# Performance work log

Measured on AMD Instinct MI355X. Metric: run time of the kernel, lower is better.

The kernel has to match this reference:

```python
import jax, jax.numpy as jnp
import numpy as np

N_DOWN, N_ABOVE, D_IN, D_OUT, FAN_IN = 50000, 100000, 256, 256, 5


def setup_inputs() -> dict:
    key = jax.random.key(0)
    ks = jax.random.split(key, 8)
    h = jax.random.normal(ks[0], (N_DOWN, D_IN), dtype=jnp.float32)
    h_above = jax.random.normal(ks[1], (N_ABOVE, D_IN), dtype=jnp.float32)  # only shape[0] used
    # idx: unique positions of the down nodes within the up-node index space
    idx = jax.random.permutation(ks[2], N_ABOVE)[:N_DOWN]
    # fixed fan-in 5: destination ids i are each node repeated 5 times (DGL bucketing order)
    i = jnp.repeat(jnp.arange(N_ABOVE), FAN_IN)
    j = jax.random.randint(ks[3], (N_ABOVE * FAN_IN,), 0, N_ABOVE)
    s1 = 1.0 / np.sqrt(D_IN * FAN_IN)
    s2 = 1.0 / np.sqrt(D_OUT)
    W1 = jax.random.uniform(ks[4], (D_IN * FAN_IN, D_OUT), jnp.float32, -s1, s1)
    b1 = jax.random.uniform(ks[5], (D_OUT,), jnp.float32, -s1, s1)
    W2 = jax.random.uniform(ks[6], (D_OUT, D_OUT), jnp.float32, -s2, s2)
    b2 = jax.random.uniform(ks[7], (D_OUT,), jnp.float32, -s2, s2)
    return {"h": h, "h_above": h_above, "idx": idx, "i": i, "j": j,
            "W1": W1, "b1": b1, "W2": W2, "b2": b2}


def reference(h, h_above, idx, i, j, W1, b1, W2, b2):
    n_above = h_above.shape[0]
    d = h.shape[1]
    # scatter down-node features into the up-node index space (new_h[idx] = h)
    new_h = jnp.zeros((n_above, d), dtype=h.dtype).at[idx].set(h)
    # gather the 5 source-node messages per destination; i = repeat(arange, 5),
    # so j grouped in blocks of 5 corresponds to each destination's mailbox.
    gathered = new_h[j].reshape(n_above, 5 * d)  # [n_above, 5*d]
    hid = jax.nn.relu(gathered @ W1 + b1)
    return hid @ W2 + b2
```

## Files before the change

kernel.cpp:

```cpp
#include <hip/hip_runtime.h>

#define N_DOWN  50000
#define N_ABOVE 100000
#define DIM     256
#define FAN     5
#define K1      1280
#define MPAD    100096

typedef __bf16 bf16x8 __attribute__((ext_vector_type(8)));
typedef float  f32x4  __attribute__((ext_vector_type(4)));

__device__ __forceinline__ unsigned short f2bf(float f) {
  unsigned u = __builtin_bit_cast(unsigned, f);
  u += 0x7FFFu + ((u >> 16) & 1u);
  return (unsigned short)(u >> 16);
}

__device__ __forceinline__ void gload16(const unsigned short* g, unsigned short* l) {
  __builtin_amdgcn_global_load_lds(
      (const __attribute__((address_space(1))) void*)g,
      (__attribute__((address_space(3))) void*)l, 16, 0, 0);
}

__global__ void k_prep_inv(int* __restrict__ inv, unsigned short* __restrict__ hbf) {
  int t = blockIdx.x * 256 + threadIdx.x;
  if (t < N_ABOVE) inv[t] = N_DOWN;
  if (t < DIM)     hbf[(size_t)N_DOWN * DIM + t] = 0;
}

__global__ void k_scatter(const int* __restrict__ idx, int* __restrict__ inv) {
  int t = blockIdx.x * 256 + threadIdx.x;
  if (t < N_DOWN) inv[idx[t]] = t;
}

__global__ void k_h2bf(const float* __restrict__ h, unsigned short* __restrict__ hbf) {
  int t = blockIdx.x * 256 + threadIdx.x;
  float4 v = ((const float4*)h)[t];
  ushort4 o;
  o.x = f2bf(v.x); o.y = f2bf(v.y); o.z = f2bf(v.z); o.w = f2bf(v.w);
  ((ushort4*)hbf)[t] = o;
}

__global__ void k_transpose_bf(const float* __restrict__ in, unsigned short* __restrict__ out,
                               int K, int N) {
  __shared__ float tile[64][65];
  int k0 = blockIdx.x * 64, n0 = blockIdx.y * 64;
  int c = threadIdx.x & 63, rb = threadIdx.x >> 6;
#pragma unroll
  for (int rr = 0; rr < 16; ++rr) {
    int row = rb + rr * 4;
    tile[row][c] = in[(size_t)(k0 + row) * N + n0 + c];
  }
  __syncthreads();
#pragma unroll
  for (int rr = 0; rr < 16; ++rr) {
    int nr = rb + rr * 4;
    out[(size_t)(n0 + nr) * K + k0 + c] = f2bf(tile[c][nr]);
  }
}

__global__ __launch_bounds__(256, 2) void k_gemm1(
    const unsigned short* __restrict__ hbf,
    const unsigned short* __restrict__ w1t,
    const float* __restrict__ b1,
    const int* __restrict__ inv,
    const int* __restrict__ jarr,
    unsigned short* __restrict__ hid)
{
  __shared__ __align__(16) unsigned short Alds[128 * 64];
  __shared__ __align__(16) unsigned short Blds[128 * 64];
  __shared__ int srcrow[128 * FAN];

  const int tid = threadIdx.x;
  const int w = tid >> 6, l = tid & 63;
  const int m0 = blockIdx.x * 128, n0 = blockIdx.y * 128;
  const int wm = w >> 1, wn = w & 1;
  const int srow = l >> 3, slot = l & 7;

  for (int e = tid; e < 128 * FAN; e += 256) {
    int row = e / FAN, rr = e - row * FAN;
    int gm = m0 + row;
    int s = N_DOWN;
    if (gm < N_ABOVE) s = inv[jarr[(size_t)gm * FAN + rr]];
    srcrow[e] = s;
  }

  f32x4 acc[4][4] = {};

  for (int t = 0; t < 20; ++t) {
    const int r = t >> 2;
    __syncthreads();
#pragma unroll
    for (int i = 0; i < 4; ++i) {
      int row = w * 32 + i * 8 + srow;
      int src = srcrow[row * FAN + r];
      int c = slot ^ (row & 7);
      gload16(hbf + ((size_t)src << 8) + ((t & 3) << 6) + (c << 3),
              Alds + (w * 32 + i * 8) * 64);
    }
#pragma unroll
    for (int i = 0; i < 4; ++i) {
      int row = w * 32 + i * 8 + srow;
      int c = slot ^ (row & 7);
      gload16(w1t + (size_t)(n0 + row) * K1 + (t << 6) + (c << 3),
              Blds + (w * 32 + i * 8) * 64);
    }
    __syncthreads();

#pragma unroll
    for (int kk = 0; kk < 2; ++kk) {
      bf16x8 af[4], bfr[4];
#pragma unroll
      for (int m = 0; m < 4; ++m) {
        int row = wm * 64 + m * 16 + (l & 15);
        int c = (kk * 4 + (l >> 4)) ^ (row & 7);
        af[m] = *(const bf16x8*)(Alds + row * 64 + c * 8);
      }
#pragma unroll
      for (int n = 0; n < 4; ++n) {
        int row = wn * 64 + n * 16 + (l & 15);
        int c = (kk * 4 + (l >> 4)) ^ (row & 7);
        bfr[n] = *(const bf16x8*)(Blds + row * 64 + c * 8);
      }
#pragma unroll
      for (int m = 0; m < 4; ++m)
#pragma unroll
        for (int n = 0; n < 4; ++n)
          acc[m][n] = __builtin_amdgcn_mfma_f32_16x16x32_bf16(af[m], bfr[n], acc[m][n], 0, 0, 0);
    }
  }

#pragma unroll
  for (int n = 0; n < 4; ++n) {
    int gn = n0 + wn * 64 + n * 16 + (l & 15);
    float bias = b1[gn];
#pragma unroll
    for (int m = 0; m < 4; ++m) {
      int gm0 = m0 + wm * 64 + m * 16 + (l >> 4) * 4;
#pragma unroll
      for (int q = 0; q < 4; ++q) {
        float v = acc[m][n][q] + bias;
        v = v > 0.f ? v : 0.f;
        hid[(size_t)(gm0 + q) * DIM + gn] = f2bf(v);
      }
    }
  }
}

__global__ __launch_bounds__(256, 2) void k_gemm2(
    const unsigned short* __restrict__ hid,
    const unsigned short* __restrict__ w2t,
    const float* __restrict__ b2,
    float* __restrict__ out)
{
  __shared__ __align__(16) unsigned short Alds[128 * 64];
  __shared__ __align__(16) unsigned short Blds[128 * 64];

  const int tid = threadIdx.x;
  const int w = tid >> 6, l = tid & 63;
  const int m0 = blockIdx.x * 128, n0 = blockIdx.y * 128;
  const int wm = w >> 1, wn = w & 1;
  const int srow = l >> 3, slot = l & 7;

  f32x4 acc[4][4] = {};

  for (int t = 0; t < 4; ++t) {
    __syncthreads();
#pragma unroll
    for (int i = 0; i < 4; ++i) {
      int row = w * 32 + i * 8 + srow;
      int c = slot ^ (row & 7);
      gload16(hid + (size_t)(m0 + row) * DIM + (t << 6) + (c << 3),
              Alds + (w * 32 + i * 8) * 64);
      gload16(w2t + (size_t)(n0 + row) * DIM + (t << 6) + (c << 3),
              Blds + (w * 32 + i * 8) * 64);
    }
    __syncthreads();

#pragma unroll
    for (int kk = 0; kk < 2; ++kk) {
      bf16x8 af[4], bfr[4];
#pragma unroll
      for (int m = 0; m < 4; ++m) {
        int row = wm * 64 + m * 16 + (l & 15);
        int c = (kk * 4 + (l >> 4)) ^ (row & 7);
        af[m] = *(const bf16x8*)(Alds + row * 64 + c * 8);
      }
#pragma unroll
      for (int n = 0; n < 4; ++n) {
        int row = wn * 64 + n * 16 + (l & 15);
        int c = (kk * 4 + (l >> 4)) ^ (row & 7);
        bfr[n] = *(const bf16x8*)(Blds + row * 64 + c * 8);
      }
#pragma unroll
      for (int m = 0; m < 4; ++m)
#pragma unroll
        for (int n = 0; n < 4; ++n)
          acc[m][n] = __builtin_amdgcn_mfma_f32_16x16x32_bf16(af[m], bfr[n], acc[m][n], 0, 0, 0);
    }
  }

#pragma unroll
  for (int n = 0; n < 4; ++n) {
    int gn = n0 + wn * 64 + n * 16 + (l & 15);
    float bias = b2[gn];
#pragma unroll
    for (int m = 0; m < 4; ++m) {
      int gm0 = m0 + wm * 64 + m * 16 + (l >> 4) * 4;
#pragma unroll
      for (int q = 0; q < 4; ++q) {
        int gm = gm0 + q;
        if (gm < N_ABOVE) out[(size_t)gm * DIM + gn] = acc[m][n][q] + bias;
      }
    }
  }
}

extern "C" void kernel_launch(void* const* d_in, const int* in_sizes, int n_in,
                              void* d_out, int out_size, void* d_ws, size_t ws_size,
                              hipStream_t stream) {
  const float* h    = (const float*)d_in[0];
  const int*   idx  = (const int*)d_in[2];
  const int*   jarr = (const int*)d_in[4];
  const float* W1   = (const float*)d_in[5];
  const float* b1   = (const float*)d_in[6];
  const float* W2   = (const float*)d_in[7];
  const float* b2   = (const float*)d_in[8];
  float* out = (float*)d_out;

  char* ws = (char*)d_ws;
  size_t off = 0;
  auto alloc = [&](size_t bytes) -> void* {
    void* p = ws + off;
    off += bytes;
    off = (off + 511) & ~(size_t)511;
    return p;
  };
  int*            inv = (int*)alloc((size_t)N_ABOVE * 4);
  unsigned short* hbf = (unsigned short*)alloc((size_t)(N_DOWN + 1) * DIM * 2);
  unsigned short* w1t = (unsigned short*)alloc((size_t)DIM * K1 * 2);
  unsigned short* w2t = (unsigned short*)alloc((size_t)DIM * DIM * 2);
  unsigned short* hid = (unsigned short*)alloc((size_t)MPAD * DIM * 2);
  if (ws_size < off) return;

  k_prep_inv<<<dim3(391), dim3(256), 0, stream>>>(inv, hbf);
  k_scatter<<<dim3(196), dim3(256), 0, stream>>>(idx, inv);
  k_h2bf<<<dim3(12500), dim3(256), 0, stream>>>(h, hbf);
  k_transpose_bf<<<dim3(K1 / 64, DIM / 64), dim3(256), 0, stream>>>(W1, w1t, K1, DIM);
  k_transpose_bf<<<dim3(DIM / 64, DIM / 64), dim3(256), 0, stream>>>(W2, w2t, DIM, DIM);
  k_gemm1<<<dim3(MPAD / 128, 2), dim3(256), 0, stream>>>(hbf, w1t, b1, inv, jarr, hid);
  k_gemm2<<<dim3(MPAD / 128, 2), dim3(256), 0, stream>>>(hid, w2t, b2, out);
}
```

Measured before the change: 142.8 us.

## Restructure gemm1 with 128x256 tiles, 512 threads and triple-buffered async pipeline

Rewrites the first GEMM so each block covers the full 256-wide output with 8 waves, which halves the number of gathers of the indexed A rows. It triple-buffers LDS and prefetches two K-tiles ahead using direct-to-LDS loads with explicit vmcnt waits. MFMA phases are interleaved with half-tile LDS reads and raised wave priority. The source indices are held in registers instead of LDS. This uses about 147KB of dynamic shared memory per block, which limits occupancy, and it relies on hand-placed waitcnt and barrier ordering for correctness.

```diff
diff --git a/kernel.cpp b/kernel.cpp
--- a/kernel.cpp
+++ b/kernel.cpp
@@ -6,6 +6,7 @@
 #define FAN     5
 #define K1      1280
 #define MPAD    100096
+#define NT      20
 
 typedef __bf16 bf16x8 __attribute__((ext_vector_type(8)));
 typedef float  f32x4  __attribute__((ext_vector_type(4)));
@@ -21,6 +22,10 @@
       (const __attribute__((address_space(1))) void*)g,
       (__attribute__((address_space(3))) void*)l, 16, 0, 0);
 }
+
+#define BAR()   __builtin_amdgcn_s_barrier()
+#define LGKM0() do { asm volatile("s_waitcnt lgkmcnt(0)" ::: "memory"); \
+                     __builtin_amdgcn_sched_barrier(0); } while (0)
 
 __global__ void k_prep_inv(int* __restrict__ inv, unsigned short* __restrict__ hbf) {
   int t = blockIdx.x * 256 + threadIdx.x;
@@ -59,7 +64,7 @@
   }
 }
 
-__global__ __launch_bounds__(256, 2) void k_gemm1(
+__global__ __launch_bounds__(512, 2) void k_gemm1(
     const unsigned short* __restrict__ hbf,
     const unsigned short* __restrict__ w1t,
     const float* __restrict__ b1,
@@ -67,81 +72,147 @@
     const int* __restrict__ jarr,
     unsigned short* __restrict__ hid)
 {
-  __shared__ __align__(16) unsigned short Alds[128 * 64];
-  __shared__ __align__(16) unsigned short Blds[128 * 64];
-  __shared__ int srcrow[128 * FAN];
+  extern __shared__ __align__(16) unsigned short smem[];
+  unsigned short* As = smem;
+  unsigned short* Bs = smem + 3 * 128 * 64;
 
   const int tid = threadIdx.x;
   const int w = tid >> 6, l = tid & 63;
-  const int m0 = blockIdx.x * 128, n0 = blockIdx.y * 128;
-  const int wm = w >> 1, wn = w & 1;
-  const int srow = l >> 3, slot = l & 7;
-
-  for (int e = tid; e < 128 * FAN; e += 256) {
-    int row = e / FAN, rr = e - row * FAN;
-    int gm = m0 + row;
-    int s = N_DOWN;
-    if (gm < N_ABOVE) s = inv[jarr[(size_t)gm * FAN + rr]];
-    srcrow[e] = s;
-  }
+  const int m0 = blockIdx.x * 128;
+  const int wm = w & 1, wn = w >> 1;
+  const int la = l >> 3, lc = l & 7;
+
+  const int rA0 = w * 16 + la;
+  const int rA1 = w * 16 + 8 + la;
+  const int cA0 = lc ^ (rA0 & 7);
+  const int cA1 = lc ^ (rA1 & 7);
+  const int rB0 = w * 32 + la,      cB0 = lc ^ (rB0 & 7);
+  const int rB1 = w * 32 + 8 + la,  cB1 = lc ^ (rB1 & 7);
+  const int rB2 = w * 32 + 16 + la, cB2 = lc ^ (rB2 & 7);
+  const int rB3 = w * 32 + 24 + la, cB3 = lc ^ (rB3 & 7);
+
+  const int gm0 = min(m0 + rA0, N_ABOVE - 1);
+  const int gm1 = min(m0 + rA1, N_ABOVE - 1);
+  const int s00 = inv[jarr[gm0 * FAN + 0]], s01 = inv[jarr[gm0 * FAN + 1]],
+            s02 = inv[jarr[gm0 * FAN + 2]], s03 = inv[jarr[gm0 * FAN + 3]],
+            s04 = inv[jarr[gm0 * FAN + 4]];
+  const int s10 = inv[jarr[gm1 * FAN + 0]], s11 = inv[jarr[gm1 * FAN + 1]],
+            s12 = inv[jarr[gm1 * FAN + 2]], s13 = inv[jarr[gm1 * FAN + 3]],
+            s14 = inv[jarr[gm1 * FAN + 4]];
+  asm volatile("s_waitcnt vmcnt(0)" ::: "memory");
+  __builtin_amdgcn_sched_barrier(0);
+
+#pragma unroll
+  for (int t = 0; t < 2; ++t) {
+    unsigned short* An = As + t * (128 * 64);
+    unsigned short* Bn = Bs + t * (256 * 64);
+    int u = t >> 2;
+    (void)u;
+    int a0 = (t == 0) ? s00 : s00;
+    int a1 = (t == 0) ? s10 : s10;
+    gload16(hbf + ((size_t)a0 << 8) + ((t & 3) << 6) + (cA0 << 3), An + (w * 2 + 0) * 512);
+    gload16(hbf + ((size_t)a1 << 8) + ((t & 3) << 6) + (cA1 << 3), An + (w * 2 + 1) * 512);
+    gload16(w1t + (size_t)rB0 * K1 + (t << 6) + (cB0 << 3), Bn + (w * 4 + 0) * 512);
+    gload16(w1t + (size_t)rB1 * K1 + (t << 6) + (cB1 << 3), Bn + (w * 4 + 1) * 512);
+    gload16(w1t + (size_t)rB2 * K1 + (t << 6) + (cB2 << 3), Bn + (w * 4 + 2) * 512);
+    gload16(w1t + (size_t)rB3 * K1 + (t << 6) + (cB3 << 3), Bn + (w * 4 + 3) * 512);
+  }
+  asm volatile("s_waitcnt vmcnt(6)" ::: "memory");
+  BAR();
 
   f32x4 acc[4][4] = {};
-
-  for (int t = 0; t < 20; ++t) {
-    const int r = t >> 2;
-    __syncthreads();
-#pragma unroll
-    for (int i = 0; i < 4; ++i) {
-      int row = w * 32 + i * 8 + srow;
-      int src = srcrow[row * FAN + r];
-      int c = slot ^ (row & 7);
-      gload16(hbf + ((size_t)src << 8) + ((t & 3) << 6) + (c << 3),
-              Alds + (w * 32 + i * 8) * 64);
-    }
-#pragma unroll
-    for (int i = 0; i < 4; ++i) {
-      int row = w * 32 + i * 8 + srow;
-      int c = slot ^ (row & 7);
-      gload16(w1t + (size_t)(n0 + row) * K1 + (t << 6) + (c << 3),
-              Blds + (w * 32 + i * 8) * 64);
-    }
-    __syncthreads();
-
-#pragma unroll
-    for (int kk = 0; kk < 2; ++kk) {
-      bf16x8 af[4], bfr[4];
-#pragma unroll
-      for (int m = 0; m < 4; ++m) {
-        int row = wm * 64 + m * 16 + (l & 15);
-        int c = (kk * 4 + (l >> 4)) ^ (row & 7);
-        af[m] = *(const bf16x8*)(Alds + row * 64 + c * 8);
-      }
-#pragma unroll
-      for (int n = 0; n < 4; ++n) {
-        int row = wn * 64 + n * 16 + (l & 15);
-        int c = (kk * 4 + (l >> 4)) ^ (row & 7);
-        bfr[n] = *(const bf16x8*)(Blds + row * 64 + c * 8);
-      }
-#pragma unroll
-      for (int m = 0; m < 4; ++m)
-#pragma unroll
-        for (int n = 0; n < 4; ++n)
-          acc[m][n] = __builtin_amdgcn_mfma_f32_16x16x32_bf16(af[m], bfr[n], acc[m][n], 0, 0, 0);
-    }
-  }
-
-#pragma unroll
-  for (int n = 0; n < 4; ++n) {
-    int gn = n0 + wn * 64 + n * 16 + (l & 15);
+  int cur = 0;
+
+  for (int t = 0; t < NT; ++t) {
+    const int t2 = t + 2;
+    const bool do_stage = (t2 < NT);
+    const int u = t2 >> 2;
+    const int sA0 = u == 0 ? s00 : u == 1 ? s01 : u == 2 ? s02 : u == 3 ? s03 : s04;
+    const int sA1 = u == 0 ? s10 : u == 1 ? s11 : u == 2 ? s12 : u == 3 ? s13 : s14;
+    unsigned short* Ab = As + cur * (128 * 64);
+    unsigned short* Bb = Bs + cur * (256 * 64);
+    int nx = cur + 2; if (nx >= 3) nx -= 3;
+    unsigned short* An = As + nx * (128 * 64);
+    unsigned short* Bn = Bs + nx * (256 * 64);
+
+    bf16x8 a0[4], b0[4];
+#pragma unroll
+    for (int mf = 0; mf < 4; ++mf) {
+      int row = wm * 64 + mf * 16 + (l & 15);
+      int p = (l >> 4) ^ (row & 7);
+      a0[mf] = *(const bf16x8*)(Ab + row * 64 + p * 8);
+    }
+#pragma unroll
+    for (int nf = 0; nf < 4; ++nf) {
+      int row = wn * 64 + nf * 16 + (l & 15);
+      int p = (l >> 4) ^ (row & 7);
+      b0[nf] = *(const bf16x8*)(Bb + row * 64 + p * 8);
+    }
+    if (do_stage) {
+      gload16(hbf + ((size_t)sA0 << 8) + ((t2 & 3) << 6) + (cA0 << 3), An + (w * 2 + 0) * 512);
+      gload16(hbf + ((size_t)sA1 << 8) + ((t2 & 3) << 6) + (cA1 << 3), An + (w * 2 + 1) * 512);
+      gload16(w1t + (size_t)rB0 * K1 + (t2 << 6) + (cB0 << 3), Bn + (w * 4 + 0) * 512);
+    }
+    BAR();
+    LGKM0();
+    __builtin_amdgcn_s_setprio(1);
+#pragma unroll
+    for (int mf = 0; mf < 4; ++mf)
+#pragma unroll
+      for (int nf = 0; nf < 4; ++nf)
+        acc[mf][nf] = __builtin_amdgcn_mfma_f32_16x16x32_bf16(a0[mf], b0[nf], acc[mf][nf], 0, 0, 0);
+    __builtin_amdgcn_s_setprio(0);
+    BAR();
+
+    bf16x8 a1[4], b1f[4];
+#pragma unroll
+    for (int mf = 0; mf < 4; ++mf) {
+      int row = wm * 64 + mf * 16 + (l & 15);
+      int p = (4 + (l >> 4)) ^ (row & 7);
+      a1[mf] = *(const bf16x8*)(Ab + row * 64 + p * 8);
+    }
+#pragma unroll
+    for (int nf = 0; nf < 4; ++nf) {
+      int row = wn * 64 + nf * 16 + (l & 15);
+      int p = (4 + (l >> 4)) ^ (row & 7);
+      b1f[nf] = *(const bf16x8*)(Bb + row * 64 + p * 8);
+    }
+    if (do_stage) {
+      gload16(w1t + (size_t)rB1 * K1 + (t2 << 6) + (cB1 << 3), Bn + (w * 4 + 1) * 512);
+      gload16(w1t + (size_t)rB2 * K1 + (t2 << 6) + (cB2 << 3), Bn + (w * 4 + 2) * 512);
+      gload16(w1t + (size_t)rB3 * K1 + (t2 << 6) + (cB3 << 3), Bn + (w * 4 + 3) * 512);
+    }
+    BAR();
+    LGKM0();
+    __builtin_amdgcn_s_setprio(1);
+#pragma unroll
+    for (int mf = 0; mf < 4; ++mf)
+#pragma unroll
+      for (int nf = 0; nf < 4; ++nf)
+        acc[mf][nf] = __builtin_amdgcn_mfma_f32_16x16x32_bf16(a1[mf], b1f[nf], acc[mf][nf], 0, 0, 0);
+    __builtin_amdgcn_s_setprio(0);
+    if (t == NT - 2) {
+      asm volatile("s_waitcnt vmcnt(0)" ::: "memory");
+    } else if (t < NT - 2) {
+      asm volatile("s_waitcnt vmcnt(6)" ::: "memory");
+    }
+    BAR();
+
+    ++cur; if (cur >= 3) cur = 0;
+  }
+
+#pragma unroll
+  for (int nf = 0; nf < 4; ++nf) {
+    int gn = wn * 64 + nf * 16 + (l & 15);
     float bias = b1[gn];
 #pragma unroll
-    for (int m = 0; m < 4; ++m) {
-      int gm0 = m0 + wm * 64 + m * 16 + (l >> 4) * 4;
+    for (int mf = 0; mf < 4; ++mf) {
+      int gr0 = m0 + wm * 64 + mf * 16 + (l >> 4) * 4;
 #pragma unroll
       for (int q = 0; q < 4; ++q) {
-        float v = acc[m][n][q] + bias;
+        float v = acc[mf][nf][q] + bias;
         v = v > 0.f ? v : 0.f;
-        hid[(size_t)(gm0 + q) * DIM + gn] = f2bf(v);
+        hid[(size_t)(gr0 + q) * DIM + gn] = f2bf(v);
       }
     }
   }
@@ -248,6 +319,7 @@
   k_h2bf<<<dim3(12500), dim3(256), 0, stream>>>(h, hbf);
   k_transpose_bf<<<dim3(K1 / 64, DIM / 64), dim3(256), 0, stream>>>(W1, w1t, K1, DIM);
   k_transpose_bf<<<dim3(DIM / 64, DIM / 64), dim3(256), 0, stream>>>(W2, w2t, DIM, DIM);
-  k_gemm1<<<dim3(MPAD / 128, 2), dim3(256), 0, stream>>>(hbf, w1t, b1, inv, jarr, hid);
+  const size_t smem1 = (size_t)(3 * 128 * 64 + 3 * 256 * 64) * sizeof(unsigned short);
+  k_gemm1<<<dim3(MPAD / 128), dim3(512), smem1, stream>>>(hbf, w1t, b1, inv, jarr, hid);
   k_gemm2<<<dim3(MPAD / 128, 2), dim3(256), 0, stream>>>(hid, w2t, b2, out);
 }
```

Measured after the change: 168.0 us. 17.7% more time.

## Restructure GEMMs into 256x256 tiles with triple-buffered LDS ring pipeline

Applied to the files above, without the earlier changes.

Both GEMM kernels now use 512-thread blocks that each compute a full 256-row by 256-column output tile, so the gathered A rows are loaded once rather than once per N-block. Global-to-LDS loads go into a three-slot ring buffer with prefetch two steps ahead, explicit vmcnt/lgkmcnt waits, raw barriers and setprio around the MFMA bursts, so loads overlap compute. The gather indices are kept in registers instead of shared memory. In exchange, register pressure rises (128 accumulator floats per thread) and the grid has half as many blocks, which may lower occupancy.

```diff
diff --git a/kernel.cpp b/kernel.cpp
--- a/kernel.cpp
+++ b/kernel.cpp
@@ -6,6 +6,9 @@
 #define FAN     5
 #define K1      1280
 #define MPAD    100096
+#define NT1     40
+#define NT2     8
+#define BUFE    8192
 
 typedef __bf16 bf16x8 __attribute__((ext_vector_type(8)));
 typedef float  f32x4  __attribute__((ext_vector_type(4)));
@@ -21,6 +24,14 @@
       (const __attribute__((address_space(1))) void*)g,
       (__attribute__((address_space(3))) void*)l, 16, 0, 0);
 }
+
+#define BAR()   __builtin_amdgcn_s_barrier()
+#define LGKM0() do { asm volatile("s_waitcnt lgkmcnt(0)" ::: "memory"); \
+                     __builtin_amdgcn_sched_barrier(0); } while (0)
+#define VMW4()  do { asm volatile("s_waitcnt vmcnt(4)" ::: "memory"); \
+                     __builtin_amdgcn_sched_barrier(0); } while (0)
+#define VMW0()  do { asm volatile("s_waitcnt vmcnt(0)" ::: "memory"); \
+                     __builtin_amdgcn_sched_barrier(0); } while (0)
 
 __global__ void k_prep_inv(int* __restrict__ inv, unsigned short* __restrict__ hbf) {
   int t = blockIdx.x * 256 + threadIdx.x;
@@ -59,7 +70,8 @@
   }
 }
 
-__global__ __launch_bounds__(256, 2) void k_gemm1(
+
+__global__ __launch_bounds__(512, 2) void k_gemm1(
     const unsigned short* __restrict__ hbf,
     const unsigned short* __restrict__ w1t,
     const float* __restrict__ b1,
@@ -67,153 +79,259 @@
     const int* __restrict__ jarr,
     unsigned short* __restrict__ hid)
 {
-  __shared__ __align__(16) unsigned short Alds[128 * 64];
-  __shared__ __align__(16) unsigned short Blds[128 * 64];
-  __shared__ int srcrow[128 * FAN];
+  extern __shared__ __align__(16) unsigned short smem[];
+  unsigned short* Aring = smem;
+  unsigned short* Bring = smem + 3 * BUFE;
 
   const int tid = threadIdx.x;
   const int w = tid >> 6, l = tid & 63;
-  const int m0 = blockIdx.x * 128, n0 = blockIdx.y * 128;
-  const int wm = w >> 1, wn = w & 1;
-  const int srow = l >> 3, slot = l & 7;
-
-  for (int e = tid; e < 128 * FAN; e += 256) {
-    int row = e / FAN, rr = e - row * FAN;
-    int gm = m0 + row;
-    int s = N_DOWN;
-    if (gm < N_ABOVE) s = inv[jarr[(size_t)gm * FAN + rr]];
-    srcrow[e] = s;
-  }
-
-  f32x4 acc[4][4] = {};
-
-  for (int t = 0; t < 20; ++t) {
-    const int r = t >> 2;
-    __syncthreads();
-#pragma unroll
-    for (int i = 0; i < 4; ++i) {
-      int row = w * 32 + i * 8 + srow;
-      int src = srcrow[row * FAN + r];
-      int c = slot ^ (row & 7);
-      gload16(hbf + ((size_t)src << 8) + ((t & 3) << 6) + (c << 3),
-              Alds + (w * 32 + i * 8) * 64);
-    }
-#pragma unroll
-    for (int i = 0; i < 4; ++i) {
-      int row = w * 32 + i * 8 + srow;
-      int c = slot ^ (row & 7);
-      gload16(w1t + (size_t)(n0 + row) * K1 + (t << 6) + (c << 3),
-              Blds + (w * 32 + i * 8) * 64);
-    }
-    __syncthreads();
-
-#pragma unroll
-    for (int kk = 0; kk < 2; ++kk) {
-      bf16x8 af[4], bfr[4];
-#pragma unroll
-      for (int m = 0; m < 4; ++m) {
-        int row = wm * 64 + m * 16 + (l & 15);
-        int c = (kk * 4 + (l >> 4)) ^ (row & 7);
-        af[m] = *(const bf16x8*)(Alds + row * 64 + c * 8);
-      }
-#pragma unroll
-      for (int n = 0; n < 4; ++n) {
-        int row = wn * 64 + n * 16 + (l & 15);
-        int c = (kk * 4 + (l >> 4)) ^ (row & 7);
-        bfr[n] = *(const bf16x8*)(Blds + row * 64 + c * 8);
-      }
-#pragma unroll
-      for (int m = 0; m < 4; ++m)
-#pragma unroll
-        for (int n = 0; n < 4; ++n)
-          acc[m][n] = __builtin_amdgcn_mfma_f32_16x16x32_bf16(af[m], bfr[n], acc[m][n], 0, 0, 0);
-    }
-  }
-
-#pragma unroll
-  for (int n = 0; n < 4; ++n) {
-    int gn = n0 + wn * 64 + n * 16 + (l & 15);
+  const int m0 = blockIdx.x * 256;
+  const int wm = w & 1, wn = w >> 1;
+
+  const int line0 = w * 16 + (l >> 3);
+  const int line1 = line0 + 8;
+  const int u0 = (l & 7) ^ (line0 & 7);
+  const int u1 = (l & 7) ^ (line1 & 7);
+  const int r0 = 2 * line0 + (u0 >> 2), kc0 = (u0 & 3) * 8;
+  const int r1 = 2 * line1 + (u1 >> 2), kc1 = (u1 & 3) * 8;
+  const int adst0 = w * 1024;
+  const int adst1 = w * 1024 + 512;
+
+  const int gm0 = min(m0 + r0, N_ABOVE - 1);
+  const int gm1 = min(m0 + r1, N_ABOVE - 1);
+  const int s00 = inv[jarr[(size_t)gm0 * FAN + 0]], s01 = inv[jarr[(size_t)gm0 * FAN + 1]],
+            s02 = inv[jarr[(size_t)gm0 * FAN + 2]], s03 = inv[jarr[(size_t)gm0 * FAN + 3]],
+            s04 = inv[jarr[(size_t)gm0 * FAN + 4]];
+  const int s10 = inv[jarr[(size_t)gm1 * FAN + 0]], s11 = inv[jarr[(size_t)gm1 * FAN + 1]],
+            s12 = inv[jarr[(size_t)gm1 * FAN + 2]], s13 = inv[jarr[(size_t)gm1 * FAN + 3]],
+            s14 = inv[jarr[(size_t)gm1 * FAN + 4]];
+
+  int aoff[8], boff[4];
+#pragma unroll
+  for (int mf = 0; mf < 8; ++mf) {
+    int row = wm * 128 + mf * 16 + (l & 15);
+    int line = row >> 1;
+    int chk = (((row & 1) << 2) | (l >> 4)) ^ (line & 7);
+    aoff[mf] = line * 64 + chk * 8;
+  }
+#pragma unroll
+  for (int nf = 0; nf < 4; ++nf) {
+    int row = wn * 64 + nf * 16 + (l & 15);
+    int line = row >> 1;
+    int chk = (((row & 1) << 2) | (l >> 4)) ^ (line & 7);
+    boff[nf] = line * 64 + chk * 8;
+  }
+
+  VMW0();
+
+#define STAGE_A1(tt, Abuf, S0, S1) do {                                          \
+    gload16(hbf + ((size_t)(S0) << 8) + (((tt) & 7) << 5) + kc0, (Abuf) + adst0);\
+    gload16(hbf + ((size_t)(S1) << 8) + (((tt) & 7) << 5) + kc1, (Abuf) + adst1);\
+  } while (0)
+#define STAGE_B1(tt, Bbuf) do {                                                  \
+    gload16(w1t + (size_t)r0 * K1 + ((tt) << 5) + kc0, (Bbuf) + adst0);          \
+    gload16(w1t + (size_t)r1 * K1 + ((tt) << 5) + kc1, (Bbuf) + adst1);          \
+  } while (0)
+
+  STAGE_A1(0, Aring, s00, s10);
+  STAGE_B1(0, Bring);
+  STAGE_A1(1, Aring + BUFE, s00, s10);
+  STAGE_B1(1, Bring + BUFE);
+  VMW4();
+  BAR();
+
+  f32x4 acc[8][4] = {};
+  int cur = 0, nx2 = 2;
+
+#pragma unroll 1
+  for (int t = 0; t < NT1; ++t) {
+    unsigned short* Ac = Aring + cur * BUFE;
+    unsigned short* Bc = Bring + cur * BUFE;
+    unsigned short* An = Aring + nx2 * BUFE;
+    unsigned short* Bn = Bring + nx2 * BUFE;
+    const int t2 = t + 2;
+    const bool do_stage = (t2 < NT1);
+    const int u = t2 >> 3;
+    const int ss0 = u == 0 ? s00 : u == 1 ? s01 : u == 2 ? s02 : u == 3 ? s03 : s04;
+    const int ss1 = u == 0 ? s10 : u == 1 ? s11 : u == 2 ? s12 : u == 3 ? s13 : s14;
+
+    bf16x8 af[4], bfr[4];
+#pragma unroll
+    for (int mf = 0; mf < 4; ++mf) af[mf] = *(const bf16x8*)(Ac + aoff[mf]);
+#pragma unroll
+    for (int nf = 0; nf < 4; ++nf) bfr[nf] = *(const bf16x8*)(Bc + boff[nf]);
+    if (do_stage) STAGE_A1(t2, An, ss0, ss1);
+    BAR();
+    LGKM0();
+    __builtin_amdgcn_s_setprio(1);
+#pragma unroll
+    for (int mf = 0; mf < 4; ++mf)
+#pragma unroll
+      for (int nf = 0; nf < 4; ++nf)
+        acc[mf][nf] = __builtin_amdgcn_mfma_f32_16x16x32_bf16(af[mf], bfr[nf], acc[mf][nf], 0, 0, 0);
+    __builtin_amdgcn_s_setprio(0);
+    BAR();
+
+#pragma unroll
+    for (int mf = 0; mf < 4; ++mf) af[mf] = *(const bf16x8*)(Ac + aoff[4 + mf]);
+    if (do_stage) STAGE_B1(t2, Bn);
+    BAR();
+    LGKM0();
+    __builtin_amdgcn_s_setprio(1);
+#pragma unroll
+    for (int mf = 0; mf < 4; ++mf)
+#pragma unroll
+      for (int nf = 0; nf < 4; ++nf)
+        acc[4 + mf][nf] = __builtin_amdgcn_mfma_f32_16x16x32_bf16(af[mf], bfr[nf], acc[4 + mf][nf], 0, 0, 0);
+    __builtin_amdgcn_s_setprio(0);
+    if (t < NT1 - 2) { VMW4(); } else if (t == NT1 - 2) { VMW0(); }
+    BAR();
+
+    cur = (cur == 2) ? 0 : cur + 1;
+    nx2 = (nx2 == 2) ? 0 : nx2 + 1;
+  }
+
+#pragma unroll
+  for (int nf = 0; nf < 4; ++nf) {
+    int gn = wn * 64 + nf * 16 + (l & 15);
     float bias = b1[gn];
 #pragma unroll
-    for (int m = 0; m < 4; ++m) {
-      int gm0 = m0 + wm * 64 + m * 16 + (l >> 4) * 4;
+    for (int mf = 0; mf < 8; ++mf) {
+      int gr0 = m0 + wm * 128 + mf * 16 + (l >> 4) * 4;
 #pragma unroll
       for (int q = 0; q < 4; ++q) {
-        float v = acc[m][n][q] + bias;
+        float v = acc[mf][nf][q] + bias;
         v = v > 0.f ? v : 0.f;
-        hid[(size_t)(gm0 + q) * DIM + gn] = f2bf(v);
+        hid[(size_t)(gr0 + q) * DIM + gn] = f2bf(v);
       }
     }
   }
-}
-
-__global__ __launch_bounds__(256, 2) void k_gemm2(
+#undef STAGE_A1
+#undef STAGE_B1
+}
+
+__global__ __launch_bounds__(512, 2) void k_gemm2(
     const unsigned short* __restrict__ hid,
     const unsigned short* __restrict__ w2t,
     const float* __restrict__ b2,
     float* __restrict__ out)
 {
-  __shared__ __align__(16) unsigned short Alds[128 * 64];
-  __shared__ __align__(16) unsigned short Blds[128 * 64];
+  extern __shared__ __align__(16) unsigned short smem[];
+  unsigned short* Aring = smem;
+  unsigned short* Bring = smem + 3 * BUFE;
 
   const int tid = threadIdx.x;
   const int w = tid >> 6, l = tid & 63;
-  const int m0 = blockIdx.x * 128, n0 = blockIdx.y * 128;
-  const int wm = w >> 1, wn = w & 1;
-  const int srow = l >> 3, slot = l & 7;
-
-  f32x4 acc[4][4] = {};
-
-  for (int t = 0; t < 4; ++t) {
-    __syncthreads();
-#pragma unroll
-    for (int i = 0; i < 4; ++i) {
-      int row = w * 32 + i * 8 + srow;
-      int c = slot ^ (row & 7);
-      gload16(hid + (size_t)(m0 + row) * DIM + (t << 6) + (c << 3),
-              Alds + (w * 32 + i * 8) * 64);
-      gload16(w2t + (size_t)(n0 + row) * DIM + (t << 6) + (c << 3),
-              Blds + (w * 32 + i * 8) * 64);
-    }
-    __syncthreads();
-
-#pragma unroll
-    for (int kk = 0; kk < 2; ++kk) {
-      bf16x8 af[4], bfr[4];
-#pragma unroll
-      for (int m = 0; m < 4; ++m) {
-        int row = wm * 64 + m * 16 + (l & 15);
-        int c = (kk * 4 + (l >> 4)) ^ (row & 7);
-        af[m] = *(const bf16x8*)(Alds + row * 64 + c * 8);
-      }
-#pragma unroll
-      for (int n = 0; n < 4; ++n) {
-        int row = wn * 64 + n * 16 + (l & 15);
-        int c = (kk * 4 + (l >> 4)) ^ (row & 7);
-        bfr[n] = *(const bf16x8*)(Blds + row * 64 + c * 8);
-      }
-#pragma unroll
-      for (int m = 0; m < 4; ++m)
-#pragma unroll
-        for (int n = 0; n < 4; ++n)
-          acc[m][n] = __builtin_amdgcn_mfma_f32_16x16x32_bf16(af[m], bfr[n], acc[m][n], 0, 0, 0);
-    }
-  }
-
-#pragma unroll
-  for (int n = 0; n < 4; ++n) {
-    int gn = n0 + wn * 64 + n * 16 + (l & 15);
+  const int m0 = blockIdx.x * 256;
+  const int wm = w & 1, wn = w >> 1;
+
+  const int line0 = w * 16 + (l >> 3);
+  const int line1 = line0 + 8;
+  const int u0 = (l & 7) ^ (line0 & 7);
+  const int u1 = (l & 7) ^ (line1 & 7);
+  const int r0 = 2 * line0 + (u0 >> 2), kc0 = (u0 & 3) * 8;
+  const int r1 = 2 * line1 + (u1 >> 2), kc1 = (u1 & 3) * 8;
+  const int adst0 = w * 1024;
+  const int adst1 = w * 1024 + 512;
+
+  int aoff[8], boff[4];
+#pragma unroll
+  for (int mf = 0; mf < 8; ++mf) {
+    int row = wm * 128 + mf * 16 + (l & 15);
+    int line = row >> 1;
+    int chk = (((row & 1) << 2) | (l >> 4)) ^ (line & 7);
+    aoff[mf] = line * 64 + chk * 8;
+  }
+#pragma unroll
+  for (int nf = 0; nf < 4; ++nf) {
+    int row = wn * 64 + nf * 16 + (l & 15);
+    int line = row >> 1;
+    int chk = (((row & 1) << 2) | (l >> 4)) ^ (line & 7);
+    boff[nf] = line * 64 + chk * 8;
+  }
+
+  VMW0();
+
+#define STAGE_A2(tt, Abuf) do {                                                       \
+    gload16(hid + (size_t)(m0 + r0) * DIM + ((tt) << 5) + kc0, (Abuf) + adst0);       \
+    gload16(hid + (size_t)(m0 + r1) * DIM + ((tt) << 5) + kc1, (Abuf) + adst1);       \
+  } while (0)
+#define STAGE_B2(tt, Bbuf) do {                                                       \
+    gload16(w2t + (size_t)r0 * DIM + ((tt) << 5) + kc0, (Bbuf) + adst0);              \
+    gload16(w2t + (size_t)r1 * DIM + ((tt) << 5) + kc1, (Bbuf) + adst1);              \
+  } while (0)
+
+  STAGE_A2(0, Aring);
+  STAGE_B2(0, Bring);
+  STAGE_A2(1, Aring + BUFE);
+  STAGE_B2(1, Bring + BUFE);
+  VMW4();
+  BAR();
+
+  f32x4 acc[8][4] = {};
+  int cur = 0, nx2 = 2;
+
+#pragma unroll 1
+  for (int t = 0; t < NT2; ++t) {
+    unsigned short* Ac = Aring + cur * BUFE;
+    unsigned short* Bc = Bring + cur * BUFE;
+    unsigned short* An = Aring + nx2 * BUFE;
+    unsigned short* Bn = Bring + nx2 * BUFE;
+    const int t2 = t + 2;
+    const bool do_stage = (t2 < NT2);
+
+    bf16x8 af[4], bfr[4];
+#pragma unroll
+    for (int mf = 0; mf < 4; ++mf) af[mf] = *(const bf16x8*)(Ac + aoff[mf]);
+#pragma unroll
+    for (int nf = 0; nf < 4; ++nf) bfr[nf] = *(const bf16x8*)(Bc + boff[nf]);
+    if (do_stage) STAGE_A2(t2, An);
+    BAR();
+    LGKM0();
+    __builtin_amdgcn_s_setprio(1);
+#pragma unroll
+    for (int mf = 0; mf < 4; ++mf)
+#pragma unroll
+      for (int nf = 0; nf < 4; ++nf)
+        acc[mf][nf] = __builtin_amdgcn_mfma_f32_16x16x32_bf16(af[mf], bfr[nf], acc[mf][nf], 0, 0, 0);
+    __builtin_amdgcn_s_setprio(0);
+    BAR();
+
+#pragma unroll
+    for (int mf = 0; mf < 4; ++mf) af[mf] = *(const bf16x8*)(Ac + aoff[4 + mf]);
+    if (do_stage) STAGE_B2(t2, Bn);
+    BAR();
+    LGKM0();
+    __builtin_amdgcn_s_setprio(1);
+#pragma unroll
+    for (int mf = 0; mf < 4; ++mf)
+#pragma unroll
+      for (int nf = 0; nf < 4; ++nf)
+        acc[4 + mf][nf] = __builtin_amdgcn_mfma_f32_16x16x32_bf16(af[mf], bfr[nf], acc[4 + mf][nf], 0, 0, 0);
+    __builtin_amdgcn_s_setprio(0);
+    if (t < NT2 - 2) { VMW4(); } else if (t == NT2 - 2) { VMW0(); }
+    BAR();
+
+    cur = (cur == 2) ? 0 : cur + 1;
+    nx2 = (nx2 == 2) ? 0 : nx2 + 1;
+  }
+
+#pragma unroll
+  for (int nf = 0; nf < 4; ++nf) {
+    int gn = wn * 64 + nf * 16 + (l & 15);
     float bias = b2[gn];
 #pragma unroll
-    for (int m = 0; m < 4; ++m) {
-      int gm0 = m0 + wm * 64 + m * 16 + (l >> 4) * 4;
+    for (int mf = 0; mf < 8; ++mf) {
+      int gr0 = m0 + wm * 128 + mf * 16 + (l >> 4) * 4;
 #pragma unroll
       for (int q = 0; q < 4; ++q) {
-        int gm = gm0 + q;
-        if (gm < N_ABOVE) out[(size_t)gm * DIM + gn] = acc[m][n][q] + bias;
+        int gm = gr0 + q;
+        if (gm < N_ABOVE) out[(size_t)gm * DIM + gn] = acc[mf][nf][q] + bias;
       }
     }
   }
+#undef STAGE_A2
+#undef STAGE_B2
 }
 
 extern "C" void kernel_launch(void* const* d_in, const int* in_sizes, int n_in,
@@ -248,6 +366,7 @@
   k_h2bf<<<dim3(12500), dim3(256), 0, stream>>>(h, hbf);
   k_transpose_bf<<<dim3(K1 / 64, DIM / 64), dim3(256), 0, stream>>>(W1, w1t, K1, DIM);
   k_transpose_bf<<<dim3(DIM / 64, DIM / 64), dim3(256), 0, stream>>>(W2, w2t, DIM, DIM);
-  k_gemm1<<<dim3(MPAD / 128, 2), dim3(256), 0, stream>>>(hbf, w1t, b1, inv, jarr, hid);
-  k_gemm2<<<dim3(MPAD / 128, 2), dim3(256), 0, stream>>>(hid, w2t, b2, out);
-}
+  const size_t smem = (size_t)(6 * BUFE) * sizeof(unsigned short);
+  k_gemm1<<<dim3(MPAD / 256), dim3(512), smem, stream>>>(hbf, w1t, b1, inv, jarr, hid);
+  k_gemm2<<<dim3(MPAD / 256), dim3(512), smem, stream>>>(hid, w2t, b2, out);
+}
```

Result: slower. 171.7 us (+20.3%).

## Fuse both MLP GEMMs into one kernel keeping hidden tile in LDS

Applied to the files above, without the earlier changes.

Merges the two GEMM kernels into a single 512-thread kernel. Each block now computes all 256 hidden columns for its 128 rows, applies bias and ReLU, and writes the bf16 hidden tile into a swizzled LDS buffer that reuses the A/B staging memory. It then runs the second GEMM from LDS, reading W2 fragments straight from global memory. This removes the round trip of the hidden activations through HBM and one kernel launch. The cost is 64KB of LDS per block, which limits occupancy, and uncached global reads of W2 inside the inner loop.

```diff
diff --git a/kernel.cpp b/kernel.cpp
--- a/kernel.cpp
+++ b/kernel.cpp
@@ -59,25 +59,29 @@
   }
 }
 
-__global__ __launch_bounds__(256, 2) void k_gemm1(
+__global__ __launch_bounds__(512, 4) void k_fused(
     const unsigned short* __restrict__ hbf,
     const unsigned short* __restrict__ w1t,
     const float* __restrict__ b1,
+    const unsigned short* __restrict__ w2t,
+    const float* __restrict__ b2,
     const int* __restrict__ inv,
     const int* __restrict__ jarr,
-    unsigned short* __restrict__ hid)
+    float* __restrict__ out)
 {
-  __shared__ __align__(16) unsigned short Alds[128 * 64];
-  __shared__ __align__(16) unsigned short Blds[128 * 64];
-  __shared__ int srcrow[128 * FAN];
+  extern __shared__ __align__(16) unsigned short smem[];
+  unsigned short* Alds = smem;
+  unsigned short* Blds = smem + 128 * 64;
+  int* srcrow = (int*)(smem + 128 * 64 + 256 * 64);
+  unsigned short* hid_lds = smem;
 
   const int tid = threadIdx.x;
   const int w = tid >> 6, l = tid & 63;
-  const int m0 = blockIdx.x * 128, n0 = blockIdx.y * 128;
-  const int wm = w >> 1, wn = w & 1;
+  const int m0 = blockIdx.x * 128;
+  const int wm = w >> 2, wn = w & 3;
   const int srow = l >> 3, slot = l & 7;
 
-  for (int e = tid; e < 128 * FAN; e += 256) {
+  for (int e = tid; e < 128 * FAN; e += 512) {
     int row = e / FAN, rr = e - row * FAN;
     int gm = m0 + row;
     int s = N_DOWN;
@@ -91,18 +95,18 @@
     const int r = t >> 2;
     __syncthreads();
 #pragma unroll
-    for (int i = 0; i < 4; ++i) {
-      int row = w * 32 + i * 8 + srow;
+    for (int i = 0; i < 2; ++i) {
+      int row = w * 16 + i * 8 + srow;
       int src = srcrow[row * FAN + r];
       int c = slot ^ (row & 7);
       gload16(hbf + ((size_t)src << 8) + ((t & 3) << 6) + (c << 3),
-              Alds + (w * 32 + i * 8) * 64);
+              Alds + (w * 16 + i * 8) * 64);
     }
 #pragma unroll
     for (int i = 0; i < 4; ++i) {
       int row = w * 32 + i * 8 + srow;
       int c = slot ^ (row & 7);
-      gload16(w1t + (size_t)(n0 + row) * K1 + (t << 6) + (c << 3),
+      gload16(w1t + (size_t)row * K1 + (t << 6) + (c << 3),
               Blds + (w * 32 + i * 8) * 64);
     }
     __syncthreads();
@@ -129,88 +133,58 @@
           acc[m][n] = __builtin_amdgcn_mfma_f32_16x16x32_bf16(af[m], bfr[n], acc[m][n], 0, 0, 0);
     }
   }
-
-#pragma unroll
-  for (int n = 0; n < 4; ++n) {
-    int gn = n0 + wn * 64 + n * 16 + (l & 15);
-    float bias = b1[gn];
-#pragma unroll
-    for (int m = 0; m < 4; ++m) {
-      int gm0 = m0 + wm * 64 + m * 16 + (l >> 4) * 4;
+  __syncthreads();
+
+#pragma unroll
+  for (int nf = 0; nf < 4; ++nf) {
+    int col = wn * 64 + nf * 16 + (l & 15);
+    float bias = b1[col];
+#pragma unroll
+    for (int mf = 0; mf < 4; ++mf) {
 #pragma unroll
       for (int q = 0; q < 4; ++q) {
-        float v = acc[m][n][q] + bias;
+        int row = wm * 64 + mf * 16 + (l >> 4) * 4 + q;
+        float v = acc[mf][nf][q] + bias;
         v = v > 0.f ? v : 0.f;
-        hid[(size_t)(gm0 + q) * DIM + gn] = f2bf(v);
-      }
-    }
-  }
-}
-
-__global__ __launch_bounds__(256, 2) void k_gemm2(
-    const unsigned short* __restrict__ hid,
-    const unsigned short* __restrict__ w2t,
-    const float* __restrict__ b2,
-    float* __restrict__ out)
-{
-  __shared__ __align__(16) unsigned short Alds[128 * 64];
-  __shared__ __align__(16) unsigned short Blds[128 * 64];
-
-  const int tid = threadIdx.x;
-  const int w = tid >> 6, l = tid & 63;
-  const int m0 = blockIdx.x * 128, n0 = blockIdx.y * 128;
-  const int wm = w >> 1, wn = w & 1;
-  const int srow = l >> 3, slot = l & 7;
-
-  f32x4 acc[4][4] = {};
-
-  for (int t = 0; t < 4; ++t) {
-    __syncthreads();
-#pragma unroll
-    for (int i = 0; i < 4; ++i) {
-      int row = w * 32 + i * 8 + srow;
-      int c = slot ^ (row & 7);
-      gload16(hid + (size_t)(m0 + row) * DIM + (t << 6) + (c << 3),
-              Alds + (w * 32 + i * 8) * 64);
-      gload16(w2t + (size_t)(n0 + row) * DIM + (t << 6) + (c << 3),
-              Blds + (w * 32 + i * 8) * 64);
-    }
-    __syncthreads();
-
-#pragma unroll
-    for (int kk = 0; kk < 2; ++kk) {
-      bf16x8 af[4], bfr[4];
-#pragma unroll
-      for (int m = 0; m < 4; ++m) {
-        int row = wm * 64 + m * 16 + (l & 15);
-        int c = (kk * 4 + (l >> 4)) ^ (row & 7);
-        af[m] = *(const bf16x8*)(Alds + row * 64 + c * 8);
-      }
-#pragma unroll
-      for (int n = 0; n < 4; ++n) {
-        int row = wn * 64 + n * 16 + (l & 15);
-        int c = (kk * 4 + (l >> 4)) ^ (row & 7);
-        bfr[n] = *(const bf16x8*)(Blds + row * 64 + c * 8);
-      }
-#pragma unroll
-      for (int m = 0; m < 4; ++m)
-#pragma unroll
-        for (int n = 0; n < 4; ++n)
-          acc[m][n] = __builtin_amdgcn_mfma_f32_16x16x32_bf16(af[m], bfr[n], acc[m][n], 0, 0, 0);
-    }
-  }
-
-#pragma unroll
-  for (int n = 0; n < 4; ++n) {
-    int gn = n0 + wn * 64 + n * 16 + (l & 15);
+        hid_lds[row * 256 + (((col >> 3) ^ (row & 7)) << 3) + (col & 7)] = f2bf(v);
+      }
+    }
+  }
+  __syncthreads();
+
+  f32x4 acc2[4][4] = {};
+#pragma unroll 1
+  for (int t2 = 0; t2 < 8; ++t2) {
+    bf16x8 af2[4], bf2[4];
+#pragma unroll
+    for (int nf = 0; nf < 4; ++nf) {
+      int nr = wn * 64 + nf * 16 + (l & 15);
+      bf2[nf] = *(const bf16x8*)(w2t + (size_t)nr * DIM + t2 * 32 + ((l >> 4) << 3));
+    }
+#pragma unroll
+    for (int mf = 0; mf < 4; ++mf) {
+      int row = wm * 64 + mf * 16 + (l & 15);
+      int g = t2 * 4 + (l >> 4);
+      af2[mf] = *(const bf16x8*)(hid_lds + row * 256 + ((g ^ (row & 7)) << 3));
+    }
+#pragma unroll
+    for (int mf = 0; mf < 4; ++mf)
+#pragma unroll
+      for (int nf = 0; nf < 4; ++nf)
+        acc2[mf][nf] = __builtin_amdgcn_mfma_f32_16x16x32_bf16(af2[mf], bf2[nf], acc2[mf][nf], 0, 0, 0);
+  }
+
+#pragma unroll
+  for (int nf = 0; nf < 4; ++nf) {
+    int gn = wn * 64 + nf * 16 + (l & 15);
     float bias = b2[gn];
 #pragma unroll
-    for (int m = 0; m < 4; ++m) {
-      int gm0 = m0 + wm * 64 + m * 16 + (l >> 4) * 4;
+    for (int mf = 0; mf < 4; ++mf) {
+      int gr0 = m0 + wm * 64 + mf * 16 + (l >> 4) * 4;
 #pragma unroll
       for (int q = 0; q < 4; ++q) {
-        int gm = gm0 + q;
-        if (gm < N_ABOVE) out[(size_t)gm * DIM + gn] = acc[m][n][q] + bias;
+        int gm = gr0 + q;
+        if (gm < N_ABOVE) out[(size_t)gm * DIM + gn] = acc2[mf][nf][q] + bias;
       }
     }
   }
@@ -240,7 +214,6 @@
   unsigned short* hbf = (unsigned short*)alloc((size_t)(N_DOWN + 1) * DIM * 2);
   unsigned short* w1t = (unsigned short*)alloc((size_t)DIM * K1 * 2);
   unsigned short* w2t = (unsigned short*)alloc((size_t)DIM * DIM * 2);
-  unsigned short* hid = (unsigned short*)alloc((size_t)MPAD * DIM * 2);
   if (ws_size < off) return;
 
   k_prep_inv<<<dim3(391), dim3(256), 0, stream>>>(inv, hbf);
@@ -248,6 +221,6 @@
   k_h2bf<<<dim3(12500), dim3(256), 0, stream>>>(h, hbf);
   k_transpose_bf<<<dim3(K1 / 64, DIM / 64), dim3(256), 0, stream>>>(W1, w1t, K1, DIM);
   k_transpose_bf<<<dim3(DIM / 64, DIM / 64), dim3(256), 0, stream>>>(W2, w2t, DIM, DIM);
-  k_gemm1<<<dim3(MPAD / 128, 2), dim3(256), 0, stream>>>(hbf, w1t, b1, inv, jarr, hid);
-  k_gemm2<<<dim3(MPAD / 128, 2), dim3(256), 0, stream>>>(hid, w2t, b2, out);
-}
+  const size_t smem = 65536;
+  k_fused<<<dim3(MPAD / 128), dim3(512), smem, stream>>>(hbf, w1t, b1, w2t, b2, inv, jarr, out);
+}
```

New measurement: 146.6 us. 2.7% more time.
